# Optimization experiments

Hardware: AMD Instinct MI355X
Metric: run time of the kernel (lower is better)

Reference implementation:

```python
import jax, jax.numpy as jnp
import numpy as np


def setup_inputs() -> dict:
    key = jax.random.key(0)
    k1, k2, k3 = jax.random.split(key, 3)
    B, S, E = 4, 8192, 1024
    x = jax.random.normal(k1, (B, S, E), dtype=jnp.float32)
    # torch nn.Linear weights have shape [out_features, in_features]
    W1 = jax.random.normal(k2, (3 * E, E), dtype=jnp.float32) * (1.0 / np.sqrt(E))
    W2 = jax.random.normal(k3, (E, E), dtype=jnp.float32) * (1.0 / np.sqrt(E))
    return {"x": x, "W1": W1, "W2": W2, "heads": 16}


def reference(x, W1, W2, heads):
    B, S, E = x.shape
    h = heads
    e = E // h
    # qkv projection: [B,S,3E] -> 'b s (n h e) -> n b h s e'
    qkv = (x @ W1.T).reshape(B, S, 3, h, e)
    qkv = jnp.transpose(qkv, (2, 0, 3, 1, 4))  # [3,B,h,S,e]
    q, k, v = qkv[0], qkv[1], qkv[2]
    # score: [B,h,e,e], softmax over last dim (c)
    score = jax.nn.softmax(jnp.einsum('bhnk,bhnc->bhkc', k / 4, v), axis=-1)
    # einsum 'bhnk,bhkc->bhnk': elementwise over k, sum over c
    attn = jax.nn.softmax(jnp.einsum('bhnk,bhkc->bhnk', q / 4, score), axis=-1)
    # 'b h s e -> b s (h e)' then linear_2
    out = jnp.transpose(attn, (0, 2, 1, 3)).reshape(B, S, E) @ W2.T
    return out
```

## Files before the change

### kernel.cpp

```cpp
#include <hip/hip_runtime.h>
#include <hip/hip_bf16.h>
#include <stdint.h>

static constexpr int MTOT = 32768;
static constexpr int KD   = 1024;
static constexpr int ND   = 1024;

static constexpr int BM = 256, BN = 256, BK = 64;
static constexpr int NT = KD / BK;
static constexpr int BUF_BYTES = 65536;
static constexpr int BOFF = 32768;
static constexpr int HALF = 16384;

typedef __bf16 bf16x8 __attribute__((ext_vector_type(8)));
typedef float  f32x4  __attribute__((ext_vector_type(4)));

__device__ __forceinline__ unsigned short f2bf_rne(float f) {
  union { float f; uint32_t u; } c; c.f = f;
  uint32_t u = c.u;
  return (unsigned short)((u + 0x7fffu + ((u >> 16) & 1u)) >> 16);
}

__global__ void cast_all(const float* __restrict__ x,
                         const float* __restrict__ W1,
                         const float* __restrict__ W2,
                         unsigned short* __restrict__ xb,
                         unsigned short* __restrict__ w1b,
                         unsigned short* __restrict__ w2b) {
  constexpr int n4x = MTOT * KD / 4;
  constexpr int n4w = KD * KD / 4;
  constexpr int total = n4x + 2 * n4w;
  int idx = blockIdx.x * blockDim.x + threadIdx.x;
  int stride = gridDim.x * blockDim.x;
  for (int i = idx; i < total; i += stride) {
    const float* s; unsigned short* d; int j;
    if (i < n4x)            { s = x;  d = xb;  j = i; }
    else if (i < n4x + n4w) { s = W1; d = w1b; j = i - n4x; }
    else                    { s = W2; d = w2b; j = i - n4x - n4w; }
    float4 v = reinterpret_cast<const float4*>(s)[j];
    ushort4 o;
    o.x = f2bf_rne(v.x); o.y = f2bf_rne(v.y);
    o.z = f2bf_rne(v.z); o.w = f2bf_rne(v.w);
    reinterpret_cast<ushort4*>(d)[j] = o;
  }
}

__device__ __forceinline__ void gload_lds16(const void* g, void* lds) {
  __builtin_amdgcn_global_load_lds(
      (const __attribute__((address_space(1))) unsigned int*)g,
      (__attribute__((address_space(3))) unsigned int*)lds, 16, 0, 0);
}

template <int SOFTMAX>
__global__ __launch_bounds__(512, 2)
void gemm8(const unsigned short* __restrict__ A,
           const unsigned short* __restrict__ Bm,
           void* __restrict__ Cout) {
  extern __shared__ __align__(16) char ldsc[];

  const int tid  = threadIdx.x;
  const int lane = tid & 63;
  const int wid  = tid >> 6;
  const int wm = wid >> 2, wn = wid & 3;
  const int fr = lane & 15, fq = lane >> 4;

  const int bid0 = blockIdx.x;
  const int bid  = ((bid0 & 7) << 6) | (bid0 >> 3);
  const int brow = (bid >> 2) * BM;
  const int bcol = (bid & 3) * BN;

  const int srow  = tid >> 3;
  const int sslot = (tid & 7) ^ (srow & 7);
  const unsigned short* gA = A  + (size_t)(brow + srow) * KD + sslot * 8;
  const unsigned short* gB = Bm + (size_t)(bcol + srow) * KD + sslot * 8;

  f32x4  acc[8][4] = {};
  bf16x8 a0[4][2], a1[4][2], b01[2][2], b23[2][2];

  auto STAGE = [&](const unsigned short* g, int h, int kt, int b, int opOff) {
    const unsigned short* gu = g + (size_t)(h * 128) * KD + kt * BK;
    char* du = ldsc + b * BUF_BYTES + opOff + h * HALF + (wid << 10);
    gload_lds16(gu, du);
    gload_lds16(gu + (size_t)64 * KD, du + 8192);
  };

  auto rdA = [&](int b, bf16x8 (*dst)[2], int mBase) {
    const char* base = ldsc + b * BUF_BYTES + wm * HALF;
    #pragma unroll
    for (int mm = 0; mm < 4; ++mm) {
      const int r = (mBase + mm) * 16 + fr;
      #pragma unroll
      for (int ks = 0; ks < 2; ++ks)
        dst[mm][ks] = *(const bf16x8*)(base + (r << 7) +
                        ((ks * 64 + fq * 16) ^ ((r & 7) << 4)));
    }
  };
  auto rdB = [&](int b, int nBase, bf16x8 (*dst)[2]) {
    const char* base = ldsc + b * BUF_BYTES + BOFF + (wn >> 1) * HALF;
    #pragma unroll
    for (int nn = 0; nn < 2; ++nn) {
      const int r = (wn & 1) * 64 + (nBase + nn) * 16 + fr;
      #pragma unroll
      for (int ks = 0; ks < 2; ++ks)
        dst[nn][ks] = *(const bf16x8*)(base + (r << 7) +
                       ((ks * 64 + fq * 16) ^ ((r & 7) << 4)));
    }
  };
  auto MFMA16 = [&](int mBase, int nBase, bf16x8 (*af)[2], bf16x8 (*bf)[2]) {
    __builtin_amdgcn_s_setprio(1);
    #pragma unroll
    for (int ks = 0; ks < 2; ++ks)
      #pragma unroll
      for (int mm = 0; mm < 4; ++mm)
        #pragma unroll
        for (int nn = 0; nn < 2; ++nn)
          acc[mBase + mm][nBase + nn] = __builtin_amdgcn_mfma_f32_16x16x32_bf16(
              af[mm][ks], bf[nn][ks], acc[mBase + mm][nBase + nn], 0, 0, 0);
    __builtin_amdgcn_s_setprio(0);
  };

  auto tileStep = [&](int T, int cur, int nxt) {
    const int tp1 = (T + 1 < NT) ? T + 1 : NT - 1;
    const int tp2 = (T + 2 < NT) ? T + 2 : NT - 1;

    rdA(cur, a1, 4);
    STAGE(gB, 0, tp1, nxt, BOFF);
    MFMA16(0, 0, a0, b01);
    __builtin_amdgcn_s_barrier();

    rdB(cur, 2, b23);
    STAGE(gB, 1, tp1, nxt, BOFF);
    MFMA16(4, 0, a1, b01);
    __builtin_amdgcn_s_barrier();

    STAGE(gA, 0, tp2, cur, 0);
    STAGE(gA, 1, tp2, cur, 0);
    asm volatile("s_waitcnt vmcnt(4)" ::: "memory");
    __builtin_amdgcn_s_barrier();
    rdB(nxt, 0, b01);
    MFMA16(4, 2, a1, b23);

    MFMA16(0, 2, a0, b23);
    rdA(nxt, a0, 0);
    __builtin_amdgcn_s_barrier();
  };

  STAGE(gA, 0, 0, 0, 0);    STAGE(gA, 1, 0, 0, 0);
  STAGE(gB, 0, 0, 0, BOFF); STAGE(gB, 1, 0, 0, BOFF);
  STAGE(gA, 0, 1, 1, 0);    STAGE(gA, 1, 1, 1, 0);
  asm volatile("s_waitcnt vmcnt(4)" ::: "memory");
  __builtin_amdgcn_s_barrier();
  rdA(0, a0, 0);
  rdB(0, 0, b01);

  for (int T = 0; T < NT; T += 2) {
    tileStep(T,     0, 1);
    tileStep(T + 1, 1, 0);
  }

  if constexpr (SOFTMAX) {
    unsigned short* attn = reinterpret_cast<unsigned short*>(Cout);
    constexpr float CEXP = 0.25f * 1.44269504088896340736f;
    #pragma unroll
    for (int m = 0; m < 8; ++m) {
      const int row = brow + wm * 128 + m * 16 + fq * 4;
      #pragma unroll
      for (int j = 0; j < 4; ++j) {
        float v0 = acc[m][0][j], v1 = acc[m][1][j];
        float v2 = acc[m][2][j], v3 = acc[m][3][j];
        float mx = fmaxf(fmaxf(v0, v1), fmaxf(v2, v3));
        #pragma unroll
        for (int s = 1; s < 16; s <<= 1) mx = fmaxf(mx, __shfl_xor(mx, s, 64));
        float p0 = exp2f((v0 - mx) * CEXP);
        float p1 = exp2f((v1 - mx) * CEXP);
        float p2 = exp2f((v2 - mx) * CEXP);
        float p3 = exp2f((v3 - mx) * CEXP);
        float sm = p0 + p1 + p2 + p3;
        #pragma unroll
        for (int s = 1; s < 16; s <<= 1) sm += __shfl_xor(sm, s, 64);
        const float inv = 1.0f / sm;
        unsigned short* dst =
            attn + (size_t)(row + j) * ND + (bcol + wn * 64 + fr);
        dst[0]  = f2bf_rne(p0 * inv);
        dst[16] = f2bf_rne(p1 * inv);
        dst[32] = f2bf_rne(p2 * inv);
        dst[48] = f2bf_rne(p3 * inv);
      }
    }
  } else {
    float* Cf = reinterpret_cast<float*>(Cout);
    char* wlds = ldsc + wid * 16384;
    #pragma unroll
    for (int h = 0; h < 2; ++h) {
      asm volatile("" ::: "memory");
      #pragma unroll
      for (int mm = 0; mm < 4; ++mm)
        #pragma unroll
        for (int n = 0; n < 4; ++n)
          #pragma unroll
          for (int j = 0; j < 4; ++j)
            *(float*)(wlds + (((mm * 16 + fq * 4 + j) << 6) + n * 16 + fr) * 4)
                = acc[4 * h + mm][n][j];
      asm volatile("s_waitcnt lgkmcnt(0)" ::: "memory");
      const int rbase = brow + wm * 128 + h * 64;
      #pragma unroll
      for (int i = 0; i < 16; ++i) {
        const int idx16 = i * 64 + lane;
        const int rl = idx16 >> 4;
        const int c4 = (idx16 & 15) << 2;
        f32x4 v = *(const f32x4*)(wlds + (size_t)idx16 * 16);
        *(f32x4*)(&Cf[(size_t)(rbase + rl) * ND + (bcol + wn * 64 + c4)]) = v;
      }
      asm volatile("s_waitcnt lgkmcnt(0)" ::: "memory");
    }
  }
}

extern "C" void kernel_launch(void* const* d_in, const int* in_sizes, int n_in,
                              void* d_out, int out_size, void* d_ws, size_t ws_size,
                              hipStream_t stream) {
  const float* x  = (const float*)d_in[0];
  const float* W1 = (const float*)d_in[1];
  const float* W2 = (const float*)d_in[2];
  float* out = (float*)d_out;

  char* ws = (char*)d_ws;
  unsigned short* xb   = (unsigned short*)(ws);
  unsigned short* w1b  = (unsigned short*)(ws + (size_t)67108864);
  unsigned short* w2b  = (unsigned short*)(ws + (size_t)69206016);
  unsigned short* attn = (unsigned short*)(ws + (size_t)71303168);

  hipFuncSetAttribute(reinterpret_cast<const void*>(gemm8<1>),
                      hipFuncAttributeMaxDynamicSharedMemorySize, 131072);
  hipFuncSetAttribute(reinterpret_cast<const void*>(gemm8<0>),
                      hipFuncAttributeMaxDynamicSharedMemorySize, 131072);

  cast_all<<<2048, 256, 0, stream>>>(x, W1, W2, xb, w1b, w2b);

  const int nblk = (MTOT / BM) * (ND / BN);
  gemm8<1><<<nblk, 512, 131072, stream>>>(xb, w1b, (void*)attn);
  gemm8<0><<<nblk, 512, 131072, stream>>>(attn, w2b, (void*)out);
}
```

Measured before the change: 191.7 us.

## Prepack weights into MFMA fragment order and load B directly to registers

The prep kernel now reorders W1 and W2 into a per-lane MFMA fragment layout, so each wave can read B operands straight from global memory into registers, double-buffered across k-tiles. B no longer goes through LDS. That halves LDS use per buffer, removes the B staging barriers and LDS reads, and reshapes the pipeline schedule. In exchange, every wave issues redundant global B loads that rely on L2/L1 hits, and the register count goes up.

```diff
diff --git a/kernel.cpp b/kernel.cpp
--- a/kernel.cpp
+++ b/kernel.cpp
@@ -8,8 +8,7 @@
 
 static constexpr int BM = 256, BN = 256, BK = 64;
 static constexpr int NT = KD / BK;
-static constexpr int BUF_BYTES = 65536;
-static constexpr int BOFF = 32768;
+static constexpr int ABUF = 32768;
 static constexpr int HALF = 16384;
 
 typedef __bf16 bf16x8 __attribute__((ext_vector_type(8)));
@@ -21,27 +20,44 @@
   return (unsigned short)((u + 0x7fffu + ((u >> 16) & 1u)) >> 16);
 }
 
-__global__ void cast_all(const float* __restrict__ x,
-                         const float* __restrict__ W1,
-                         const float* __restrict__ W2,
-                         unsigned short* __restrict__ xb,
-                         unsigned short* __restrict__ w1b,
-                         unsigned short* __restrict__ w2b) {
+__global__ void prep(const float* __restrict__ x,
+                     const float* __restrict__ W1,
+                     const float* __restrict__ W2,
+                     unsigned short* __restrict__ xb,
+                     unsigned short* __restrict__ w1p,
+                     unsigned short* __restrict__ w2p) {
   constexpr int n4x = MTOT * KD / 4;
-  constexpr int n4w = KD * KD / 4;
-  constexpr int total = n4x + 2 * n4w;
-  int idx = blockIdx.x * blockDim.x + threadIdx.x;
-  int stride = gridDim.x * blockDim.x;
-  for (int i = idx; i < total; i += stride) {
-    const float* s; unsigned short* d; int j;
-    if (i < n4x)            { s = x;  d = xb;  j = i; }
-    else if (i < n4x + n4w) { s = W1; d = w1b; j = i - n4x; }
-    else                    { s = W2; d = w2b; j = i - n4x - n4w; }
-    float4 v = reinterpret_cast<const float4*>(s)[j];
+  constexpr int nChunk = (KD >> 4) * NT * 2 * 64;
+  const int idx = blockIdx.x * blockDim.x + threadIdx.x;
+  const int stride = gridDim.x * blockDim.x;
+  for (int i = idx; i < n4x; i += stride) {
+    float4 v = reinterpret_cast<const float4*>(x)[i];
     ushort4 o;
     o.x = f2bf_rne(v.x); o.y = f2bf_rne(v.y);
     o.z = f2bf_rne(v.z); o.w = f2bf_rne(v.w);
-    reinterpret_cast<ushort4*>(d)[j] = o;
+    reinterpret_cast<ushort4*>(xb)[i] = o;
+  }
+  for (int i = idx; i < 2 * nChunk; i += stride) {
+    const int m = (i >= nChunk) ? 1 : 0;
+    const int c = i - m * nChunk;
+    const float* W = m ? W2 : W1;
+    unsigned short* P = m ? w2p : w1p;
+    const int lane = c & 63;
+    const int ks   = (c >> 6) & 1;
+    const int kt   = (c >> 7) & 15;
+    const int n16  = c >> 11;
+    const int row  = n16 * 16 + (lane & 15);
+    const int k    = kt * 64 + ks * 32 + (lane >> 4) * 8;
+    const float* s = W + (size_t)row * KD + k;
+    float4 v0 = reinterpret_cast<const float4*>(s)[0];
+    float4 v1 = reinterpret_cast<const float4*>(s)[1];
+    ushort4 o0, o1;
+    o0.x = f2bf_rne(v0.x); o0.y = f2bf_rne(v0.y);
+    o0.z = f2bf_rne(v0.z); o0.w = f2bf_rne(v0.w);
+    o1.x = f2bf_rne(v1.x); o1.y = f2bf_rne(v1.y);
+    o1.z = f2bf_rne(v1.z); o1.w = f2bf_rne(v1.w);
+    reinterpret_cast<ushort4*>(P + (size_t)c * 8)[0] = o0;
+    reinterpret_cast<ushort4*>(P + (size_t)c * 8)[1] = o1;
   }
 }
 
@@ -54,7 +70,7 @@
 template <int SOFTMAX>
 __global__ __launch_bounds__(512, 2)
 void gemm8(const unsigned short* __restrict__ A,
-           const unsigned short* __restrict__ Bm,
+           const unsigned short* __restrict__ Bp,
            void* __restrict__ Cout) {
   extern __shared__ __align__(16) char ldsc[];
 
@@ -71,21 +87,21 @@
 
   const int srow  = tid >> 3;
   const int sslot = (tid & 7) ^ (srow & 7);
-  const unsigned short* gA = A  + (size_t)(brow + srow) * KD + sslot * 8;
-  const unsigned short* gB = Bm + (size_t)(bcol + srow) * KD + sslot * 8;
+  const unsigned short* gA = A + (size_t)(brow + srow) * KD + sslot * 8;
 
   f32x4  acc[8][4] = {};
-  bf16x8 a0[4][2], a1[4][2], b01[2][2], b23[2][2];
-
-  auto STAGE = [&](const unsigned short* g, int h, int kt, int b, int opOff) {
-    const unsigned short* gu = g + (size_t)(h * 128) * KD + kt * BK;
-    char* du = ldsc + b * BUF_BYTES + opOff + h * HALF + (wid << 10);
+  bf16x8 a0[4][2], a1[4][2];
+  bf16x8 b01A[2][2], b23A[2][2], b01B[2][2], b23B[2][2];
+
+  auto STAGE = [&](int h, int kt, int b) {
+    const unsigned short* gu = gA + (size_t)(h * 128) * KD + kt * BK;
+    char* du = ldsc + b * ABUF + h * HALF + (wid << 10);
     gload_lds16(gu, du);
     gload_lds16(gu + (size_t)64 * KD, du + 8192);
   };
 
   auto rdA = [&](int b, bf16x8 (*dst)[2], int mBase) {
-    const char* base = ldsc + b * BUF_BYTES + wm * HALF;
+    const char* base = ldsc + b * ABUF + wm * HALF;
     #pragma unroll
     for (int mm = 0; mm < 4; ++mm) {
       const int r = (mBase + mm) * 16 + fr;
@@ -95,15 +111,15 @@
                         ((ks * 64 + fq * 16) ^ ((r & 7) << 4)));
     }
   };
-  auto rdB = [&](int b, int nBase, bf16x8 (*dst)[2]) {
-    const char* base = ldsc + b * BUF_BYTES + BOFF + (wn >> 1) * HALF;
+  auto gldB = [&](int kt, int nBase, bf16x8 (*dst)[2]) {
     #pragma unroll
     for (int nn = 0; nn < 2; ++nn) {
-      const int r = (wn & 1) * 64 + (nBase + nn) * 16 + fr;
-      #pragma unroll
-      for (int ks = 0; ks < 2; ++ks)
-        dst[nn][ks] = *(const bf16x8*)(base + (r << 7) +
-                       ((ks * 64 + fq * 16) ^ ((r & 7) << 4)));
+      const int n16 = (bcol >> 4) + (wn << 2) + nBase + nn;
+      #pragma unroll
+      for (int ks = 0; ks < 2; ++ks) {
+        const size_t c = (((size_t)(n16 * 16 + kt) << 1) + ks) * 64 + lane;
+        dst[nn][ks] = *(const bf16x8*)(Bp + c * 8);
+      }
     }
   };
   auto MFMA16 = [&](int mBase, int nBase, bf16x8 (*af)[2], bf16x8 (*bf)[2]) {
@@ -119,43 +135,40 @@
     __builtin_amdgcn_s_setprio(0);
   };
 
-  auto tileStep = [&](int T, int cur, int nxt) {
+  auto tileStep = [&](int T, int cur, int nxt,
+                      bf16x8 (*bC01)[2], bf16x8 (*bC23)[2],
+                      bf16x8 (*bN01)[2], bf16x8 (*bN23)[2]) {
     const int tp1 = (T + 1 < NT) ? T + 1 : NT - 1;
     const int tp2 = (T + 2 < NT) ? T + 2 : NT - 1;
 
     rdA(cur, a1, 4);
-    STAGE(gB, 0, tp1, nxt, BOFF);
-    MFMA16(0, 0, a0, b01);
+    gldB(tp1, 0, bN01);
+    MFMA16(0, 0, a0, bC01);
+
+    gldB(tp1, 2, bN23);
+    MFMA16(4, 0, a1, bC01);
     __builtin_amdgcn_s_barrier();
 
-    rdB(cur, 2, b23);
-    STAGE(gB, 1, tp1, nxt, BOFF);
-    MFMA16(4, 0, a1, b01);
+    STAGE(0, tp2, cur);
+    STAGE(1, tp2, cur);
+    MFMA16(4, 2, a1, bC23);
+
+    asm volatile("s_waitcnt vmcnt(12)" ::: "memory");
     __builtin_amdgcn_s_barrier();
-
-    STAGE(gA, 0, tp2, cur, 0);
-    STAGE(gA, 1, tp2, cur, 0);
-    asm volatile("s_waitcnt vmcnt(4)" ::: "memory");
-    __builtin_amdgcn_s_barrier();
-    rdB(nxt, 0, b01);
-    MFMA16(4, 2, a1, b23);
-
-    MFMA16(0, 2, a0, b23);
+    MFMA16(0, 2, a0, bC23);
     rdA(nxt, a0, 0);
-    __builtin_amdgcn_s_barrier();
-  };
-
-  STAGE(gA, 0, 0, 0, 0);    STAGE(gA, 1, 0, 0, 0);
-  STAGE(gB, 0, 0, 0, BOFF); STAGE(gB, 1, 0, 0, BOFF);
-  STAGE(gA, 0, 1, 1, 0);    STAGE(gA, 1, 1, 1, 0);
-  asm volatile("s_waitcnt vmcnt(4)" ::: "memory");
+  };
+
+  STAGE(0, 0, 0); STAGE(1, 0, 0);
+  STAGE(0, 1, 1); STAGE(1, 1, 1);
+  gldB(0, 0, b01A); gldB(0, 2, b23A);
+  asm volatile("s_waitcnt vmcnt(12)" ::: "memory");
   __builtin_amdgcn_s_barrier();
   rdA(0, a0, 0);
-  rdB(0, 0, b01);
 
   for (int T = 0; T < NT; T += 2) {
-    tileStep(T,     0, 1);
-    tileStep(T + 1, 1, 0);
+    tileStep(T,     0, 1, b01A, b23A, b01B, b23B);
+    tileStep(T + 1, 1, 0, b01B, b23B, b01A, b23A);
   }
 
   if constexpr (SOFTMAX) {
@@ -226,8 +239,8 @@
 
   char* ws = (char*)d_ws;
   unsigned short* xb   = (unsigned short*)(ws);
-  unsigned short* w1b  = (unsigned short*)(ws + (size_t)67108864);
-  unsigned short* w2b  = (unsigned short*)(ws + (size_t)69206016);
+  unsigned short* w1p  = (unsigned short*)(ws + (size_t)67108864);
+  unsigned short* w2p  = (unsigned short*)(ws + (size_t)69206016);
   unsigned short* attn = (unsigned short*)(ws + (size_t)71303168);
 
   hipFuncSetAttribute(reinterpret_cast<const void*>(gemm8<1>),
@@ -235,9 +248,9 @@
   hipFuncSetAttribute(reinterpret_cast<const void*>(gemm8<0>),
                       hipFuncAttributeMaxDynamicSharedMemorySize, 131072);
 
-  cast_all<<<2048, 256, 0, stream>>>(x, W1, W2, xb, w1b, w2b);
+  prep<<<2048, 256, 0, stream>>>(x, W1, W2, xb, w1p, w2p);
 
   const int nblk = (MTOT / BM) * (ND / BN);
-  gemm8<1><<<nblk, 512, 131072, stream>>>(xb, w1b, (void*)attn);
-  gemm8<0><<<nblk, 512, 131072, stream>>>(attn, w2b, (void*)out);
-}
+  gemm8<1><<<nblk, 512, 131072, stream>>>(xb, w1p, (void*)attn);
+  gemm8<0><<<nblk, 512, 131072, stream>>>(attn, w2p, (void*)out);
+}
```

Result: slower. 333.4 us (+73.9%).
